# Performance work log

Measured on AMD Instinct MI355X. Metric: run time of the kernel, lower is better.

Reference implementation:

```python
import jax, jax.numpy as jnp
import numpy as np

B, D, C, Q = 4096, 128, 1000, 65536
PROTO_M = 0.99
EPS = 1e-12


def _l2norm(x, axis=-1):
    n = jnp.sqrt(jnp.sum(x * x, axis=axis, keepdims=True))
    return x / jnp.maximum(n, EPS)


def setup_inputs() -> dict:
    key = jax.random.key(0)
    ks = jax.random.split(key, 7)
    q = _l2norm(jax.random.normal(ks[0], (B, D), dtype=jnp.float32))
    k = _l2norm(jax.random.normal(ks[1], (B, D), dtype=jnp.float32))
    classfy_logits = jax.random.normal(ks[2], (B, C), dtype=jnp.float32)
    plabel = jax.random.uniform(ks[3], (B, C), dtype=jnp.float32)
    prototypes = _l2norm(jax.random.normal(ks[4], (C, D), dtype=jnp.float32))
    queue = _l2norm(jax.random.normal(ks[5], (Q, D), dtype=jnp.float32))
    queue_pseudo = jax.random.randint(ks[6], (Q,), 0, C).astype(jnp.float32)
    return {
        "q": q, "k": k, "classfy_logits": classfy_logits, "plabel": plabel,
        "prototypes": prototypes, "queue": queue, "queue_pseudo": queue_pseudo,
        "ptr": 0,
    }


def reference(q, k, classfy_logits, plabel, prototypes, queue, queue_pseudo, ptr):
    m = PROTO_M
    # classifier softmax (encoder head output)
    classfy_out = jax.nn.softmax(classfy_logits, axis=1)          # [B, C]
    # cluster logits against OLD prototypes (mm happens before EMA update)
    logits_prot = jnp.matmul(q, prototypes.T)                     # [B, C]
    cluster_out = jax.nn.softmax(logits_prot, axis=1)
    # pseudo labels from partial-label-masked scores
    pseudo_labels = jnp.argmax(classfy_out * plabel, axis=1)      # [B] int
    # --- vectorized order-dependent scatter-EMA prototype update ---
    # sequential: proto[l_i] = m*proto[l_i] + (1-m)*q_i  for i = 0..B-1
    # closed form: proto[c]*m^{n_c} + sum_i (1-m)*m^{(#later samples with same label)} q_i
    onehot = (pseudo_labels[:, None] == jnp.arange(C)[None, :])   # [B, C] bool
    counts = jnp.sum(onehot, axis=0)                              # [C] n_c
    rank = jnp.take_along_axis(jnp.cumsum(onehot.astype(jnp.int32), axis=0),
                               pseudo_labels[:, None], axis=1)[:, 0] - 1  # [B]
    n_l = counts[pseudo_labels]                                   # [B]
    w = (1.0 - m) * jnp.power(jnp.float32(m), (n_l - 1 - rank).astype(jnp.float32))
    scatter = jnp.zeros_like(prototypes).at[pseudo_labels].add(w[:, None] * q)
    decay = jnp.power(jnp.float32(m), counts.astype(jnp.float32))[:, None]
    new_prototypes = _l2norm(prototypes * decay + scatter, axis=1)
    # --- MoCo queue enqueue/dequeue (contrastive bank uses OLD queue) ---
    cont_features = jnp.concatenate([q, k, queue], axis=0)        # [2B+Q, D]
    pl_f = pseudo_labels.astype(jnp.float32)
    cont_labels = jnp.concatenate([pl_f, pl_f, queue_pseudo], axis=0)
    new_queue = jax.lax.dynamic_update_slice(queue, k, (ptr, 0))
    new_queue_pseudo = jax.lax.dynamic_update_slice(queue_pseudo, pl_f, (ptr,))
    new_ptr = (ptr + q.shape[0]) % queue.shape[0]
    return (classfy_out, cluster_out, cont_features, cont_labels,
            new_prototypes, new_queue, new_queue_pseudo, new_ptr)
```

## Files before the change

kernel.cpp:

```cpp
#include <hip/hip_runtime.h>
#include <hip/hip_bf16.h>
#include <math.h>

#define Bn 4096
#define Dn 128
#define Cn 1000
#define Qn 65536
#define CPAD 1024

typedef __attribute__((ext_vector_type(8))) short short8v;
typedef __attribute__((ext_vector_type(4))) float f32x4;

__device__ inline float waveMaxF(float v) {
    for (int o = 32; o; o >>= 1) v = fmaxf(v, __shfl_down(v, o));
    return v;
}
__device__ inline float waveSumF(float v) {
    for (int o = 32; o; o >>= 1) v += __shfl_down(v, o);
    return v;
}

__global__ __launch_bounds__(256) void k_phase1(
    const float* __restrict__ logits, const float* __restrict__ plabel,
    const float* __restrict__ q, const float* __restrict__ proto,
    const float* __restrict__ kk, const float* __restrict__ queue,
    const int* __restrict__ ptrp,
    float* __restrict__ out_cls, int* __restrict__ labels,
    __hip_bfloat16* __restrict__ qb, __hip_bfloat16* __restrict__ pb,
    float* __restrict__ out_feat, float* __restrict__ out_queue)
{
    int bid = blockIdx.x, t = threadIdx.x;
    int r3 = bid % 3;

    if (r3 == 2) {
        int cidx = bid / 3;
        int p = *ptrp;
        int pc = p < 0 ? 0 : (p > Qn - Bn ? Qn - Bn : p);
        const long long QD = (long long)Bn * Dn;
        const long long n4 = (2 * QD + (long long)Qn * Dn) / 4;
        const long long stride = 2048LL * 256;
        for (long long i = (long long)cidx * 256 + t; i < n4; i += stride) {
            long long off = i * 4;
            if (off < QD) {
                *(float4*)(out_feat + off) = *(const float4*)(q + off);
            } else if (off < 2 * QD) {
                *(float4*)(out_feat + off) = *(const float4*)(kk + off - QD);
            } else {
                long long qoff = off - 2 * QD;
                float4 v = *(const float4*)(queue + qoff);
                *(float4*)(out_feat + off) = v;
                int row = (int)(qoff >> 7);
                int col = (int)(qoff & 127);
                unsigned rr = (unsigned)(row - pc);
                if (rr < (unsigned)Bn) v = *(const float4*)(kk + (long long)rr * Dn + col);
                *(float4*)(out_queue + qoff) = v;
            }
        }
        return;
    }

    int row = (bid / 3) * 2 + r3;
    __shared__ float sh[8];
    __shared__ int   shi[4];

    {
        const int NQ = Bn * Dn;
        const int NP = CPAD * Dn;
        if (t < 160) {
            int i = row * 160 + t;
            if (i < NQ) qb[i] = __float2bfloat16(q[i]);
            else {
                int j = i - NQ;
                if (j < NP) pb[j] = __float2bfloat16(j < Cn * Dn ? proto[j] : 0.f);
            }
        }
    }

    bool act = t < 250;
    float vv[4];
    if (act) {
        float4 v4 = ((const float4*)(logits + (long long)row * Cn))[t];
        vv[0] = v4.x; vv[1] = v4.y; vv[2] = v4.z; vv[3] = v4.w;
    } else {
        vv[0] = vv[1] = vv[2] = vv[3] = -INFINITY;
    }
    int lane = t & 63, wid = t >> 6;

    float mx = fmaxf(fmaxf(vv[0], vv[1]), fmaxf(vv[2], vv[3]));
    mx = waveMaxF(mx);
    if (lane == 0) sh[wid] = mx;
    __syncthreads();
    if (t == 0) {
        float m = sh[0];
        for (int i = 1; i < 4; ++i) m = fmaxf(m, sh[i]);
        sh[4] = m;
    }
    __syncthreads();
    mx = sh[4];

    float s = 0.f;
#pragma unroll
    for (int j = 0; j < 4; ++j) {
        vv[j] = act ? expf(vv[j] - mx) : 0.f;
        s += vv[j];
    }
    s = waveSumF(s);
    if (lane == 0) sh[wid] = s;
    __syncthreads();
    if (t == 0) {
        float ss = 0.f;
        for (int i = 0; i < 4; ++i) ss += sh[i];
        sh[5] = ss;
    }
    __syncthreads();
    float inv = 1.f / sh[5];

    float bv = -INFINITY; int bi = Cn;
    if (act) {
        float4 p4 = ((const float4*)(plabel + (long long)row * Cn))[t];
        float o0 = vv[0] * inv, o1 = vv[1] * inv, o2 = vv[2] * inv, o3 = vv[3] * inv;
        ((float4*)(out_cls + (long long)row * Cn))[t] = make_float4(o0, o1, o2, o3);
        float pr[4] = {o0 * p4.x, o1 * p4.y, o2 * p4.z, o3 * p4.w};
#pragma unroll
        for (int j = 0; j < 4; ++j) {
            if (pr[j] > bv) { bv = pr[j]; bi = t * 4 + j; }
        }
    }
    for (int o = 32; o; o >>= 1) {
        float ov = __shfl_down(bv, o);
        int   oi = __shfl_down(bi, o);
        if (ov > bv || (ov == bv && oi < bi)) { bv = ov; bi = oi; }
    }
    __syncthreads();
    if (lane == 0) { sh[wid] = bv; shi[wid] = bi; }
    __syncthreads();
    if (t == 0) {
        float fb = sh[0]; int fi = shi[0];
        for (int i = 1; i < 4; ++i)
            if (sh[i] > fb || (sh[i] == fb && shi[i] < fi)) { fb = sh[i]; fi = shi[i]; }
        labels[row] = fi;
    }
}

__global__ __launch_bounds__(256) void k_phase2(
    const __hip_bfloat16* __restrict__ qb, const __hip_bfloat16* __restrict__ pb,
    const float* __restrict__ proto, const float* __restrict__ q,
    const int* __restrict__ lbl, const float* __restrict__ qps,
    const int* __restrict__ ptrp,
    float* __restrict__ outC, float* __restrict__ outp,
    float* __restrict__ out_lab, float* __restrict__ out_qps,
    float* __restrict__ out_ptr)
{
    __shared__ __align__(16) char smem[32800];
    int bid = blockIdx.x, t = threadIdx.x;

    if (bid < 256) {
        float (*red)[4] = (float (*)[4])smem;
        int lane = t & 63, w = t >> 6;
        int la = lane & 15, lk = lane >> 4;
        int row0 = bid * 16;

        f32x4 acc[16];
#pragma unroll
        for (int j = 0; j < 16; ++j) acc[j] = (f32x4){0.f, 0.f, 0.f, 0.f};

        const short* A = (const short*)qb + (long long)(row0 + la) * Dn;
        const short* Bp = (const short*)pb;
#pragma unroll
        for (int kc = 0; kc < Dn; kc += 32) {
            short8v a = *(const short8v*)(A + kc + lk * 8);
#pragma unroll
            for (int j = 0; j < 16; ++j) {
                int prow = w * 256 + j * 16 + la;
                short8v b = *(const short8v*)(Bp + (long long)prow * Dn + kc + lk * 8);
                acc[j] = __builtin_amdgcn_mfma_f32_16x16x32_bf16(a, b, acc[j], 0, 0, 0);
            }
        }

        float m[4];
#pragma unroll
        for (int rg = 0; rg < 4; ++rg) {
            float v = -INFINITY;
#pragma unroll
            for (int j = 0; j < 16; ++j) {
                int col = w * 256 + j * 16 + la;
                if (col < Cn) v = fmaxf(v, acc[j][rg]);
            }
#pragma unroll
            for (int o = 1; o < 16; o <<= 1) v = fmaxf(v, __shfl_xor(v, o));
            m[rg] = v;
        }
        if (la == 0) {
#pragma unroll
            for (int rg = 0; rg < 4; ++rg) red[lk * 4 + rg][w] = m[rg];
        }
        __syncthreads();
#pragma unroll
        for (int rg = 0; rg < 4; ++rg) {
            int r = lk * 4 + rg;
            m[rg] = fmaxf(fmaxf(red[r][0], red[r][1]), fmaxf(red[r][2], red[r][3]));
        }
        __syncthreads();

        float s[4];
#pragma unroll
        for (int rg = 0; rg < 4; ++rg) {
            float v = 0.f;
#pragma unroll
            for (int j = 0; j < 16; ++j) {
                int col = w * 256 + j * 16 + la;
                float e = (col < Cn) ? expf(acc[j][rg] - m[rg]) : 0.f;
                acc[j][rg] = e;
                v += e;
            }
#pragma unroll
            for (int o = 1; o < 16; o <<= 1) v += __shfl_xor(v, o);
            s[rg] = v;
        }
        if (la == 0) {
#pragma unroll
            for (int rg = 0; rg < 4; ++rg) red[lk * 4 + rg][w] = s[rg];
        }
        __syncthreads();
#pragma unroll
        for (int rg = 0; rg < 4; ++rg) {
            int r = lk * 4 + rg;
            s[rg] = 1.f / (red[r][0] + red[r][1] + red[r][2] + red[r][3]);
        }

#pragma unroll
        for (int j = 0; j < 16; ++j) {
            int col = w * 256 + j * 16 + la;
            if (col < Cn) {
                int rowb = row0 + lk * 4;
#pragma unroll
                for (int rg = 0; rg < 4; ++rg)
                    outC[(long long)(rowb + rg) * Cn + col] = acc[j][rg] * s[rg];
            }
        }
    } else if (bid < 756) {
        int* sl = (int*)smem;
        unsigned short* list0 = (unsigned short*)(smem + 16384);
        unsigned short* list1 = list0 + 4096;
        int* nm = (int*)(smem + 32768);
        float* shh = (float*)(smem + 32776);

        int h = t >> 7, tt = t & 127;
        int c = (bid - 256) * 2 + h;

#pragma unroll
        for (int u = 0; u < 4; ++u) {
            int base = (u * 256 + t) * 4;
            *(int4*)(sl + base) = *(const int4*)(lbl + base);
        }
        if (t == 0)   nm[0] = 0;
        if (t == 128) nm[1] = 0;
        __syncthreads();

        int wv = t >> 6;
        if ((wv & 1) == 0) {
            int hh = wv >> 1;
            int ln = t & 63;
            int cc = (bid - 256) * 2 + hh;
            unsigned short* lst = hh ? list1 : list0;
            int n = 0;
            for (int jj = 0; jj < Bn / 64; ++jj) {
                unsigned long long mask = __ballot(sl[jj * 64 + ln] == cc);
                if (ln == 0) {
                    while (mask) {
                        int b = __builtin_ctzll(mask);
                        lst[n++] = (unsigned short)(jj * 64 + b);
                        mask &= mask - 1;
                    }
                }
            }
            if (ln == 0) nm[hh] = n;
        }
        __syncthreads();

        int n = nm[h];
        unsigned short* lst = h ? list1 : list0;
        float acc = proto[(long long)c * Dn + tt];
        for (int mi = 0; mi < n; ++mi)
            acc = 0.99f * acc + 0.01f * q[(long long)lst[mi] * Dn + tt];

        float ss = waveSumF(acc * acc);
        if ((t & 63) == 0) shh[t >> 6] = ss;
        __syncthreads();
        float nn = sqrtf(shh[h * 2] + shh[h * 2 + 1]);
        outp[(long long)c * Dn + tt] = acc / fmaxf(nn, 1e-12f);
    } else {
        int gid = (bid - 756) * 256 + t;
        const int NL = 2 * Bn + Qn;
        int p = *ptrp;
        int pc = p < 0 ? 0 : (p > Qn - Bn ? Qn - Bn : p);
        if (gid < NL) {
            float v;
            if (gid < Bn)          v = (float)lbl[gid];
            else if (gid < 2 * Bn) v = (float)lbl[gid - Bn];
            else                   v = qps[gid - 2 * Bn];
            out_lab[gid] = v;
        }
        int j = gid - NL;
        if (j >= 0 && j < Qn) {
            unsigned rr = (unsigned)(j - pc);
            out_qps[j] = (rr < (unsigned)Bn) ? (float)lbl[rr] : qps[j];
        }
        if (gid == NL + Qn) out_ptr[0] = (float)((p + Bn) % Qn);
    }
}

extern "C" void kernel_launch(void* const* d_in, const int* in_sizes, int n_in,
                              void* d_out, int out_size, void* d_ws, size_t ws_size,
                              hipStream_t stream)
{
    const float* q     = (const float*)d_in[0];
    const float* kk    = (const float*)d_in[1];
    const float* cl    = (const float*)d_in[2];
    const float* plab  = (const float*)d_in[3];
    const float* proto = (const float*)d_in[4];
    const float* queue = (const float*)d_in[5];
    const float* qps   = (const float*)d_in[6];
    const int*   ptrp  = (const int*)d_in[7];

    float* out = (float*)d_out;
    const long long O_CLU  = 4096000;
    const long long O_FEAT = 8192000;
    const long long O_LAB  = 17629184;
    const long long O_PROT = 17702912;
    const long long O_QUE  = 17830912;
    const long long O_QPS  = 26219520;
    const long long O_PTR  = 26285056;

    char* ws = (char*)d_ws;
    int*   lbl = (int*)(ws + 0);
    __hip_bfloat16* qb = (__hip_bfloat16*)(ws + 1048576);
    __hip_bfloat16* pb = (__hip_bfloat16*)(ws + 2097152);

    k_phase1<<<6144, 256, 0, stream>>>(cl, plab, q, proto, kk, queue, ptrp,
                                       out, lbl, qb, pb, out + O_FEAT, out + O_QUE);
    k_phase2<<<1301, 256, 0, stream>>>(qb, pb, proto, q, lbl, qps, ptrp,
                                       out + O_CLU, out + O_PROT,
                                       out + O_LAB, out + O_QPS, out + O_PTR);
}
```

Before: 49.42 us.

## Fuse cluster GEMM-softmax into phase1 with inline bf16 conversion and nontemporal I/O

```diff
diff --git a/kernel.cpp b/kernel.cpp
--- a/kernel.cpp
+++ b/kernel.cpp
@@ -6,10 +6,10 @@
 #define Dn 128
 #define Cn 1000
 #define Qn 65536
-#define CPAD 1024
 
 typedef __attribute__((ext_vector_type(8))) short short8v;
 typedef __attribute__((ext_vector_type(4))) float f32x4;
+typedef __attribute__((ext_vector_type(4))) float f4v;
 
 __device__ inline float waveMaxF(float v) {
     for (int o = 32; o; o >>= 1) v = fmaxf(v, __shfl_down(v, o));
@@ -18,6 +18,11 @@
 __device__ inline float waveSumF(float v) {
     for (int o = 32; o; o >>= 1) v += __shfl_down(v, o);
     return v;
+}
+__device__ inline short f2bf(float x) {
+    union { __hip_bfloat16 h; short s; } u;
+    u.h = __float2bfloat16(x);
+    return u.s;
 }
 
 __global__ __launch_bounds__(256) void k_phase1(
@@ -26,14 +31,14 @@
     const float* __restrict__ kk, const float* __restrict__ queue,
     const int* __restrict__ ptrp,
     float* __restrict__ out_cls, int* __restrict__ labels,
-    __hip_bfloat16* __restrict__ qb, __hip_bfloat16* __restrict__ pb,
+    float* __restrict__ outC,
     float* __restrict__ out_feat, float* __restrict__ out_queue)
 {
     int bid = blockIdx.x, t = threadIdx.x;
-    int r3 = bid % 3;
-
-    if (r3 == 2) {
-        int cidx = bid / 3;
+    int g = bid / 25, s = bid % 25;
+
+    if (s >= 16 && s < 24) {
+        int cidx = g * 8 + (s - 16);
         int p = *ptrp;
         int pc = p < 0 ? 0 : (p > Qn - Bn ? Qn - Bn : p);
         const long long QD = (long long)Bn * Dn;
@@ -42,44 +47,133 @@
         for (long long i = (long long)cidx * 256 + t; i < n4; i += stride) {
             long long off = i * 4;
             if (off < QD) {
-                *(float4*)(out_feat + off) = *(const float4*)(q + off);
+                f4v v = *(const f4v*)(q + off);
+                __builtin_nontemporal_store(v, (f4v*)(out_feat + off));
             } else if (off < 2 * QD) {
-                *(float4*)(out_feat + off) = *(const float4*)(kk + off - QD);
+                f4v v = *(const f4v*)(kk + off - QD);
+                __builtin_nontemporal_store(v, (f4v*)(out_feat + off));
             } else {
                 long long qoff = off - 2 * QD;
-                float4 v = *(const float4*)(queue + qoff);
-                *(float4*)(out_feat + off) = v;
+                f4v v = __builtin_nontemporal_load((const f4v*)(queue + qoff));
+                __builtin_nontemporal_store(v, (f4v*)(out_feat + off));
                 int row = (int)(qoff >> 7);
                 int col = (int)(qoff & 127);
                 unsigned rr = (unsigned)(row - pc);
-                if (rr < (unsigned)Bn) v = *(const float4*)(kk + (long long)rr * Dn + col);
-                *(float4*)(out_queue + qoff) = v;
+                if (rr < (unsigned)Bn) v = *(const f4v*)(kk + (long long)rr * Dn + col);
+                __builtin_nontemporal_store(v, (f4v*)(out_queue + qoff));
             }
         }
         return;
     }
 
-    int row = (bid / 3) * 2 + r3;
+    if (s == 24) {
+        __shared__ float red[16][4];
+        int lane = t & 63, w = t >> 6;
+        int la = lane & 15, lk = lane >> 4;
+        int row0 = g * 16;
+
+        f32x4 acc[16];
+#pragma unroll
+        for (int j = 0; j < 16; ++j) acc[j] = (f32x4){0.f, 0.f, 0.f, 0.f};
+
+        const float* A0 = q + (long long)(row0 + la) * Dn;
+#pragma unroll
+        for (int kc = 0; kc < Dn; kc += 32) {
+            short8v a;
+            {
+                f4v f0 = *(const f4v*)(A0 + kc + lk * 8);
+                f4v f1 = *(const f4v*)(A0 + kc + lk * 8 + 4);
+                a[0] = f2bf(f0.x); a[1] = f2bf(f0.y); a[2] = f2bf(f0.z); a[3] = f2bf(f0.w);
+                a[4] = f2bf(f1.x); a[5] = f2bf(f1.y); a[6] = f2bf(f1.z); a[7] = f2bf(f1.w);
+            }
+#pragma unroll
+            for (int j = 0; j < 16; ++j) {
+                int prow = w * 256 + j * 16 + la;
+                short8v b = {0, 0, 0, 0, 0, 0, 0, 0};
+                if (prow < Cn) {
+                    const float* Bp0 = proto + (long long)prow * Dn + kc + lk * 8;
+                    f4v f0 = *(const f4v*)Bp0;
+                    f4v f1 = *(const f4v*)(Bp0 + 4);
+                    b[0] = f2bf(f0.x); b[1] = f2bf(f0.y); b[2] = f2bf(f0.z); b[3] = f2bf(f0.w);
+                    b[4] = f2bf(f1.x); b[5] = f2bf(f1.y); b[6] = f2bf(f1.z); b[7] = f2bf(f1.w);
+                }
+                acc[j] = __builtin_amdgcn_mfma_f32_16x16x32_bf16(a, b, acc[j], 0, 0, 0);
+            }
+        }
+
+        float m[4];
+#pragma unroll
+        for (int rg = 0; rg < 4; ++rg) {
+            float v = -INFINITY;
+#pragma unroll
+            for (int j = 0; j < 16; ++j) {
+                int col = w * 256 + j * 16 + la;
+                if (col < Cn) v = fmaxf(v, acc[j][rg]);
+            }
+#pragma unroll
+            for (int o = 1; o < 16; o <<= 1) v = fmaxf(v, __shfl_xor(v, o));
+            m[rg] = v;
+        }
+        if (la == 0) {
+#pragma unroll
+            for (int rg = 0; rg < 4; ++rg) red[lk * 4 + rg][w] = m[rg];
+        }
+        __syncthreads();
+#pragma unroll
+        for (int rg = 0; rg < 4; ++rg) {
+            int r = lk * 4 + rg;
+            m[rg] = fmaxf(fmaxf(red[r][0], red[r][1]), fmaxf(red[r][2], red[r][3]));
+        }
+        __syncthreads();
+
+        float sm[4];
+#pragma unroll
+        for (int rg = 0; rg < 4; ++rg) {
+            float v = 0.f;
+#pragma unroll
+            for (int j = 0; j < 16; ++j) {
+                int col = w * 256 + j * 16 + la;
+                float e = (col < Cn) ? expf(acc[j][rg] - m[rg]) : 0.f;
+                acc[j][rg] = e;
+                v += e;
+            }
+#pragma unroll
+            for (int o = 1; o < 16; o <<= 1) v += __shfl_xor(v, o);
+            sm[rg] = v;
+        }
+        if (la == 0) {
+#pragma unroll
+            for (int rg = 0; rg < 4; ++rg) red[lk * 4 + rg][w] = sm[rg];
+        }
+        __syncthreads();
+#pragma unroll
+        for (int rg = 0; rg < 4; ++rg) {
+            int r = lk * 4 + rg;
+            sm[rg] = 1.f / (red[r][0] + red[r][1] + red[r][2] + red[r][3]);
+        }
+
+#pragma unroll
+        for (int j = 0; j < 16; ++j) {
+            int col = w * 256 + j * 16 + la;
+            if (col < Cn) {
+                int rowb = row0 + lk * 4;
+#pragma unroll
+                for (int rg = 0; rg < 4; ++rg)
+                    __builtin_nontemporal_store(acc[j][rg] * sm[rg],
+                        outC + (long long)(rowb + rg) * Cn + col);
+            }
+        }
+        return;
+    }
+
+    int row = g * 16 + s;
     __shared__ float sh[8];
     __shared__ int   shi[4];
-
-    {
-        const int NQ = Bn * Dn;
-        const int NP = CPAD * Dn;
-        if (t < 160) {
-            int i = row * 160 + t;
-            if (i < NQ) qb[i] = __float2bfloat16(q[i]);
-            else {
-                int j = i - NQ;
-                if (j < NP) pb[j] = __float2bfloat16(j < Cn * Dn ? proto[j] : 0.f);
-            }
-        }
-    }
 
     bool act = t < 250;
     float vv[4];
     if (act) {
-        float4 v4 = ((const float4*)(logits + (long long)row * Cn))[t];
+        f4v v4 = __builtin_nontemporal_load((const f4v*)(logits + (long long)row * Cn) + t);
         vv[0] = v4.x; vv[1] = v4.y; vv[2] = v4.z; vv[3] = v4.w;
     } else {
         vv[0] = vv[1] = vv[2] = vv[3] = -INFINITY;
@@ -98,14 +192,14 @@
     __syncthreads();
     mx = sh[4];
 
-    float s = 0.f;
+    float ssum = 0.f;
 #pragma unroll
     for (int j = 0; j < 4; ++j) {
         vv[j] = act ? expf(vv[j] - mx) : 0.f;
-        s += vv[j];
-    }
-    s = waveSumF(s);
-    if (lane == 0) sh[wid] = s;
+        ssum += vv[j];
+    }
+    ssum = waveSumF(ssum);
+    if (lane == 0) sh[wid] = ssum;
     __syncthreads();
     if (t == 0) {
         float ss = 0.f;
@@ -117,9 +211,10 @@
 
     float bv = -INFINITY; int bi = Cn;
     if (act) {
-        float4 p4 = ((const float4*)(plabel + (long long)row * Cn))[t];
+        f4v p4 = __builtin_nontemporal_load((const f4v*)(plabel + (long long)row * Cn) + t);
         float o0 = vv[0] * inv, o1 = vv[1] * inv, o2 = vv[2] * inv, o3 = vv[3] * inv;
-        ((float4*)(out_cls + (long long)row * Cn))[t] = make_float4(o0, o1, o2, o3);
+        f4v o4 = {o0, o1, o2, o3};
+        __builtin_nontemporal_store(o4, (f4v*)(out_cls + (long long)row * Cn) + t);
         float pr[4] = {o0 * p4.x, o1 * p4.y, o2 * p4.z, o3 * p4.w};
 #pragma unroll
         for (int j = 0; j < 4; ++j) {
@@ -143,102 +238,17 @@
 }
 
 __global__ __launch_bounds__(256) void k_phase2(
-    const __hip_bfloat16* __restrict__ qb, const __hip_bfloat16* __restrict__ pb,
     const float* __restrict__ proto, const float* __restrict__ q,
     const int* __restrict__ lbl, const float* __restrict__ qps,
     const int* __restrict__ ptrp,
-    float* __restrict__ outC, float* __restrict__ outp,
+    float* __restrict__ outp,
     float* __restrict__ out_lab, float* __restrict__ out_qps,
     float* __restrict__ out_ptr)
 {
     __shared__ __align__(16) char smem[32800];
     int bid = blockIdx.x, t = threadIdx.x;
 
-    if (bid < 256) {
-        float (*red)[4] = (float (*)[4])smem;
-        int lane = t & 63, w = t >> 6;
-        int la = lane & 15, lk = lane >> 4;
-        int row0 = bid * 16;
-
-        f32x4 acc[16];
-#pragma unroll
-        for (int j = 0; j < 16; ++j) acc[j] = (f32x4){0.f, 0.f, 0.f, 0.f};
-
-        const short* A = (const short*)qb + (long long)(row0 + la) * Dn;
-        const short* Bp = (const short*)pb;
-#pragma unroll
-        for (int kc = 0; kc < Dn; kc += 32) {
-            short8v a = *(const short8v*)(A + kc + lk * 8);
-#pragma unroll
-            for (int j = 0; j < 16; ++j) {
-                int prow = w * 256 + j * 16 + la;
-                short8v b = *(const short8v*)(Bp + (long long)prow * Dn + kc + lk * 8);
-                acc[j] = __builtin_amdgcn_mfma_f32_16x16x32_bf16(a, b, acc[j], 0, 0, 0);
-            }
-        }
-
-        float m[4];
-#pragma unroll
-        for (int rg = 0; rg < 4; ++rg) {
-            float v = -INFINITY;
-#pragma unroll
-            for (int j = 0; j < 16; ++j) {
-                int col = w * 256 + j * 16 + la;
-                if (col < Cn) v = fmaxf(v, acc[j][rg]);
-            }
-#pragma unroll
-            for (int o = 1; o < 16; o <<= 1) v = fmaxf(v, __shfl_xor(v, o));
-            m[rg] = v;
-        }
-        if (la == 0) {
-#pragma unroll
-            for (int rg = 0; rg < 4; ++rg) red[lk * 4 + rg][w] = m[rg];
-        }
-        __syncthreads();
-#pragma unroll
-        for (int rg = 0; rg < 4; ++rg) {
-            int r = lk * 4 + rg;
-            m[rg] = fmaxf(fmaxf(red[r][0], red[r][1]), fmaxf(red[r][2], red[r][3]));
-        }
-        __syncthreads();
-
-        float s[4];
-#pragma unroll
-        for (int rg = 0; rg < 4; ++rg) {
-            float v = 0.f;
-#pragma unroll
-            for (int j = 0; j < 16; ++j) {
-                int col = w * 256 + j * 16 + la;
-                float e = (col < Cn) ? expf(acc[j][rg] - m[rg]) : 0.f;
-                acc[j][rg] = e;
-                v += e;
-            }
-#pragma unroll
-            for (int o = 1; o < 16; o <<= 1) v += __shfl_xor(v, o);
-            s[rg] = v;
-        }
-        if (la == 0) {
-#pragma unroll
-            for (int rg = 0; rg < 4; ++rg) red[lk * 4 + rg][w] = s[rg];
-        }
-        __syncthreads();
-#pragma unroll
-        for (int rg = 0; rg < 4; ++rg) {
-            int r = lk * 4 + rg;
-            s[rg] = 1.f / (red[r][0] + red[r][1] + red[r][2] + red[r][3]);
-        }
-
-#pragma unroll
-        for (int j = 0; j < 16; ++j) {
-            int col = w * 256 + j * 16 + la;
-            if (col < Cn) {
-                int rowb = row0 + lk * 4;
-#pragma unroll
-                for (int rg = 0; rg < 4; ++rg)
-                    outC[(long long)(rowb + rg) * Cn + col] = acc[j][rg] * s[rg];
-            }
-        }
-    } else if (bid < 756) {
+    if (bid < 500) {
         int* sl = (int*)smem;
         unsigned short* list0 = (unsigned short*)(smem + 16384);
         unsigned short* list1 = list0 + 4096;
@@ -246,7 +256,7 @@
         float* shh = (float*)(smem + 32776);
 
         int h = t >> 7, tt = t & 127;
-        int c = (bid - 256) * 2 + h;
+        int c = bid * 2 + h;
 
 #pragma unroll
         for (int u = 0; u < 4; ++u) {
@@ -261,7 +271,7 @@
         if ((wv & 1) == 0) {
             int hh = wv >> 1;
             int ln = t & 63;
-            int cc = (bid - 256) * 2 + hh;
+            int cc = bid * 2 + hh;
             unsigned short* lst = hh ? list1 : list0;
             int n = 0;
             for (int jj = 0; jj < Bn / 64; ++jj) {
@@ -290,7 +300,7 @@
         float nn = sqrtf(shh[h * 2] + shh[h * 2 + 1]);
         outp[(long long)c * Dn + tt] = acc / fmaxf(nn, 1e-12f);
     } else {
-        int gid = (bid - 756) * 256 + t;
+        int gid = (bid - 500) * 256 + t;
         const int NL = 2 * Bn + Qn;
         int p = *ptrp;
         int pc = p < 0 ? 0 : (p > Qn - Bn ? Qn - Bn : p);
@@ -333,13 +343,12 @@
     const long long O_PTR  = 26285056;
 
     char* ws = (char*)d_ws;
-    int*   lbl = (int*)(ws + 0);
-    __hip_bfloat16* qb = (__hip_bfloat16*)(ws + 1048576);
-    __hip_bfloat16* pb = (__hip_bfloat16*)(ws + 2097152);
-
-    k_phase1<<<6144, 256, 0, stream>>>(cl, plab, q, proto, kk, queue, ptrp,
-                                       out, lbl, qb, pb, out + O_FEAT, out + O_QUE);
-    k_phase2<<<1301, 256, 0, stream>>>(qb, pb, proto, q, lbl, qps, ptrp,
-                                       out + O_CLU, out + O_PROT,
+    int* lbl = (int*)(ws + 0);
+
+    k_phase1<<<6400, 256, 0, stream>>>(cl, plab, q, proto, kk, queue, ptrp,
+                                       out, lbl, out + O_CLU,
+                                       out + O_FEAT, out + O_QUE);
+    k_phase2<<<1045, 256, 0, stream>>>(proto, q, lbl, qps, ptrp,
+                                       out + O_PROT,
                                        out + O_LAB, out + O_QPS, out + O_PTR);
 }
```

After: 98.37 us. 99.0% more time.

## Map one softmax row per wavefront and vectorize bf16 conversion in phase1

Applied to the files above, without the earlier changes.

```diff
diff --git a/kernel.cpp b/kernel.cpp
--- a/kernel.cpp
+++ b/kernel.cpp
@@ -9,15 +9,26 @@
 #define CPAD 1024
 
 typedef __attribute__((ext_vector_type(8))) short short8v;
+typedef __attribute__((ext_vector_type(4))) short short4v;
 typedef __attribute__((ext_vector_type(4))) float f32x4;
-
-__device__ inline float waveMaxF(float v) {
-    for (int o = 32; o; o >>= 1) v = fmaxf(v, __shfl_down(v, o));
+typedef __attribute__((ext_vector_type(4))) float f4v;
+
+__device__ inline float waveAllMaxF(float v) {
+    for (int o = 32; o; o >>= 1) v = fmaxf(v, __shfl_xor(v, o));
+    return v;
+}
+__device__ inline float waveAllSumF(float v) {
+    for (int o = 32; o; o >>= 1) v += __shfl_xor(v, o);
     return v;
 }
 __device__ inline float waveSumF(float v) {
     for (int o = 32; o; o >>= 1) v += __shfl_down(v, o);
     return v;
+}
+__device__ inline short f2bf(float x) {
+    union { __hip_bfloat16 h; short s; } u;
+    u.h = __float2bfloat16(x);
+    return u.s;
 }
 
 __global__ __launch_bounds__(256) void k_phase1(
@@ -30,10 +41,10 @@
     float* __restrict__ out_feat, float* __restrict__ out_queue)
 {
     int bid = blockIdx.x, t = threadIdx.x;
-    int r3 = bid % 3;
-
-    if (r3 == 2) {
-        int cidx = bid / 3;
+    int g = bid / 3, s = bid % 3;
+
+    if (s != 0) {
+        int cidx = g * 2 + (s - 1);
         int p = *ptrp;
         int pc = p < 0 ? 0 : (p > Qn - Bn ? Qn - Bn : p);
         const long long QD = (long long)Bn * Dn;
@@ -42,104 +53,88 @@
         for (long long i = (long long)cidx * 256 + t; i < n4; i += stride) {
             long long off = i * 4;
             if (off < QD) {
-                *(float4*)(out_feat + off) = *(const float4*)(q + off);
+                *(f4v*)(out_feat + off) = *(const f4v*)(q + off);
             } else if (off < 2 * QD) {
-                *(float4*)(out_feat + off) = *(const float4*)(kk + off - QD);
+                *(f4v*)(out_feat + off) = *(const f4v*)(kk + off - QD);
             } else {
                 long long qoff = off - 2 * QD;
-                float4 v = *(const float4*)(queue + qoff);
-                *(float4*)(out_feat + off) = v;
+                f4v v = *(const f4v*)(queue + qoff);
+                *(f4v*)(out_feat + off) = v;
                 int row = (int)(qoff >> 7);
                 int col = (int)(qoff & 127);
                 unsigned rr = (unsigned)(row - pc);
-                if (rr < (unsigned)Bn) v = *(const float4*)(kk + (long long)rr * Dn + col);
-                *(float4*)(out_queue + qoff) = v;
+                if (rr < (unsigned)Bn) v = *(const f4v*)(kk + (long long)rr * Dn + col);
+                *(f4v*)(out_queue + qoff) = v;
             }
         }
         return;
     }
 
-    int row = (bid / 3) * 2 + r3;
-    __shared__ float sh[8];
-    __shared__ int   shi[4];
-
-    {
-        const int NQ = Bn * Dn;
-        const int NP = CPAD * Dn;
-        if (t < 160) {
-            int i = row * 160 + t;
-            if (i < NQ) qb[i] = __float2bfloat16(q[i]);
-            else {
-                int j = i - NQ;
-                if (j < NP) pb[j] = __float2bfloat16(j < Cn * Dn ? proto[j] : 0.f);
-            }
-        }
-    }
-
-    bool act = t < 250;
-    float vv[4];
-    if (act) {
-        float4 v4 = ((const float4*)(logits + (long long)row * Cn))[t];
-        vv[0] = v4.x; vv[1] = v4.y; vv[2] = v4.z; vv[3] = v4.w;
-    } else {
-        vv[0] = vv[1] = vv[2] = vv[3] = -INFINITY;
-    }
+    if (t < 160) {
+        int idx4 = g * 160 + t;
+        if (idx4 < 131072) {
+            f4v v = *(const f4v*)(q + (long long)idx4 * 4);
+            short4v o = {f2bf(v.x), f2bf(v.y), f2bf(v.z), f2bf(v.w)};
+            *(short4v*)((short*)qb + (long long)idx4 * 4) = o;
+        } else {
+            int j4 = idx4 - 131072;
+            short4v o = {0, 0, 0, 0};
+            if (j4 < 32000) {
+                f4v v = *(const f4v*)(proto + (long long)j4 * 4);
+                o = (short4v){f2bf(v.x), f2bf(v.y), f2bf(v.z), f2bf(v.w)};
+            }
+            *(short4v*)((short*)pb + (long long)j4 * 4) = o;
+        }
+    }
+
     int lane = t & 63, wid = t >> 6;
-
-    float mx = fmaxf(fmaxf(vv[0], vv[1]), fmaxf(vv[2], vv[3]));
-    mx = waveMaxF(mx);
-    if (lane == 0) sh[wid] = mx;
-    __syncthreads();
-    if (t == 0) {
-        float m = sh[0];
-        for (int i = 1; i < 4; ++i) m = fmaxf(m, sh[i]);
-        sh[4] = m;
-    }
-    __syncthreads();
-    mx = sh[4];
-
-    float s = 0.f;
+    int row = g * 4 + wid;
+    const float* x = logits + (long long)row * Cn;
+
+    float vv[16];
+    float mx = -INFINITY;
 #pragma unroll
     for (int j = 0; j < 4; ++j) {
-        vv[j] = act ? expf(vv[j] - mx) : 0.f;
-        s += vv[j];
-    }
-    s = waveSumF(s);
-    if (lane == 0) sh[wid] = s;
-    __syncthreads();
-    if (t == 0) {
-        float ss = 0.f;
-        for (int i = 0; i < 4; ++i) ss += sh[i];
-        sh[5] = ss;
-    }
-    __syncthreads();
-    float inv = 1.f / sh[5];
+        int f4i = lane + j * 64;
+        f4v v = (f4v){-INFINITY, -INFINITY, -INFINITY, -INFINITY};
+        if (f4i < 250) v = *(const f4v*)(x + f4i * 4);
+        vv[j * 4 + 0] = v.x; vv[j * 4 + 1] = v.y;
+        vv[j * 4 + 2] = v.z; vv[j * 4 + 3] = v.w;
+        mx = fmaxf(mx, fmaxf(fmaxf(v.x, v.y), fmaxf(v.z, v.w)));
+    }
+    mx = waveAllMaxF(mx);
+
+    float ssum = 0.f;
+#pragma unroll
+    for (int u = 0; u < 16; ++u) {
+        vv[u] = expf(vv[u] - mx);
+        ssum += vv[u];
+    }
+    ssum = waveAllSumF(ssum);
+    float inv = 1.f / ssum;
 
     float bv = -INFINITY; int bi = Cn;
-    if (act) {
-        float4 p4 = ((const float4*)(plabel + (long long)row * Cn))[t];
-        float o0 = vv[0] * inv, o1 = vv[1] * inv, o2 = vv[2] * inv, o3 = vv[3] * inv;
-        ((float4*)(out_cls + (long long)row * Cn))[t] = make_float4(o0, o1, o2, o3);
-        float pr[4] = {o0 * p4.x, o1 * p4.y, o2 * p4.z, o3 * p4.w};
-#pragma unroll
-        for (int j = 0; j < 4; ++j) {
-            if (pr[j] > bv) { bv = pr[j]; bi = t * 4 + j; }
+#pragma unroll
+    for (int j = 0; j < 4; ++j) {
+        int f4i = lane + j * 64;
+        if (f4i < 250) {
+            float o0 = vv[j * 4 + 0] * inv, o1 = vv[j * 4 + 1] * inv;
+            float o2 = vv[j * 4 + 2] * inv, o3 = vv[j * 4 + 3] * inv;
+            *((f4v*)(out_cls + (long long)row * Cn) + f4i) = (f4v){o0, o1, o2, o3};
+            f4v p4 = *((const f4v*)(plabel + (long long)row * Cn) + f4i);
+            float pr[4] = {o0 * p4.x, o1 * p4.y, o2 * p4.z, o3 * p4.w};
+#pragma unroll
+            for (int jj = 0; jj < 4; ++jj) {
+                if (pr[jj] > bv) { bv = pr[jj]; bi = f4i * 4 + jj; }
+            }
         }
     }
     for (int o = 32; o; o >>= 1) {
-        float ov = __shfl_down(bv, o);
-        int   oi = __shfl_down(bi, o);
+        float ov = __shfl_xor(bv, o);
+        int   oi = __shfl_xor(bi, o);
         if (ov > bv || (ov == bv && oi < bi)) { bv = ov; bi = oi; }
     }
-    __syncthreads();
-    if (lane == 0) { sh[wid] = bv; shi[wid] = bi; }
-    __syncthreads();
-    if (t == 0) {
-        float fb = sh[0]; int fi = shi[0];
-        for (int i = 1; i < 4; ++i)
-            if (sh[i] > fb || (sh[i] == fb && shi[i] < fi)) { fb = sh[i]; fi = shi[i]; }
-        labels[row] = fi;
-    }
+    if (lane == 0) labels[row] = bi;
 }
 
 __global__ __launch_bounds__(256) void k_phase2(
@@ -337,7 +332,7 @@
     __hip_bfloat16* qb = (__hip_bfloat16*)(ws + 1048576);
     __hip_bfloat16* pb = (__hip_bfloat16*)(ws + 2097152);
 
-    k_phase1<<<6144, 256, 0, stream>>>(cl, plab, q, proto, kk, queue, ptrp,
+    k_phase1<<<3072, 256, 0, stream>>>(cl, plab, q, proto, kk, queue, ptrp,
                                        out, lbl, qb, pb, out + O_FEAT, out + O_QUE);
     k_phase2<<<1301, 256, 0, stream>>>(qb, pb, proto, q, lbl, qps, ptrp,
                                        out + O_CLU, out + O_PROT,
```

New measurement: 49.23 us. Within noise of the previous version (-0.4%).
